# Performance work log

Hardware: AMD Instinct MI355X
Metric: run time of the kernel (lower is better)

Reference implementation:

```python
import jax, jax.numpy as jnp
import numpy as np

N = 50000          # total_nodes (B*N diagonal-stacked graphs)
E = 800000         # total edges (avg degree 16)
HID = 128          # hidden_size
HEADS = 8          # num_heads


def setup_inputs() -> dict:
    key = jax.random.key(0)
    ks = jax.random.split(key, 10)
    s = 1.0 / np.sqrt(HID)
    x = jax.random.normal(ks[0], (N, HID), jnp.float32)
    edge_index = jax.random.randint(ks[1], (2, E), 0, N, dtype=jnp.int32).astype(jnp.int64)
    Wq = jax.random.normal(ks[2], (HID, HID), jnp.float32) * s
    bq = jax.random.normal(ks[3], (HID,), jnp.float32) * 0.01
    Wk = jax.random.normal(ks[4], (HID, HID), jnp.float32) * s
    bk = jax.random.normal(ks[5], (HID,), jnp.float32) * 0.01
    Wv = jax.random.normal(ks[6], (HID, HID), jnp.float32) * s
    bv = jax.random.normal(ks[7], (HID,), jnp.float32) * 0.01
    Wo = jax.random.normal(ks[8], (HID, HID), jnp.float32) * s
    bo = jax.random.normal(ks[9], (HID,), jnp.float32) * 0.01
    return {"x": x, "edge_index": edge_index, "total_nodes": N,
            "Wq": Wq, "bq": bq, "Wk": Wk, "bk": bk,
            "Wv": Wv, "bv": bv, "Wo": Wo, "bo": bo}


def reference(x, edge_index, total_nodes, Wq, bq, Wk, bk, Wv, bv, Wo, bo):
    H = HEADS
    D = HID // HEADS
    scale = D ** (-0.5)
    # torch Linear: y = x @ W.T + b
    Q = (x @ Wq.T + bq).reshape(-1, H, D)   # (N, H, D)
    K = (x @ Wk.T + bk).reshape(-1, H, D)
    V = (x @ Wv.T + bv).reshape(-1, H, D)
    src = edge_index[0]
    dst = edge_index[1]
    # edge-wise dot-product scores: (E, H)
    scores = jnp.einsum('ehd,ehd->eh', Q[dst], K[src]) * scale
    # scatter-softmax over edges sharing the same dst node
    mx = jax.ops.segment_max(scores, dst, num_segments=total_nodes)      # (N, H)
    ex = jnp.exp(scores - mx[dst])                                        # (E, H)
    se = jax.ops.segment_sum(ex, dst, num_segments=total_nodes)          # (N, H)
    attn = ex / (se[dst] + 1e-12)                                         # (E, H)
    # weighted message aggregation
    msg = attn[..., None] * V[src]                                        # (E, H, D)
    out = jax.ops.segment_sum(msg, dst, num_segments=total_nodes)        # (N, H, D)
    out = out.reshape(total_nodes, HID)
    return out @ Wo.T + bo
```

## Files before the change

### kernel.cpp

```cpp
#include <hip/hip_runtime.h>
#include <math.h>

#define NNODES 50000
#define NEDGES 800000
#define HIDDEN 128
#define NH 8
#define HD 16
#define CAP 64
#define NPART 8
#define PART_SZ 6250
#define SCAT_BPP 128
#define SCAT_BLOCKS (NPART * SCAT_BPP)
#define QKV_BLOCKS 782

typedef __bf16 bf16x8 __attribute__((ext_vector_type(8)));
typedef float  f32x4  __attribute__((ext_vector_type(4)));

__device__ inline unsigned short f2b(float f) {
    unsigned u = __float_as_uint(f);
    unsigned r = (u + 0x7fffu + ((u >> 16) & 1u)) >> 16;
    return (unsigned short)r;
}

__device__ inline bf16x8 ld_a8(const float* __restrict__ p) {
    float4 a = *(const float4*)p;
    float4 b = *(const float4*)(p + 4);
    bf16x8 r;
    r[0] = (__bf16)a.x; r[1] = (__bf16)a.y; r[2] = (__bf16)a.z; r[3] = (__bf16)a.w;
    r[4] = (__bf16)b.x; r[5] = (__bf16)b.y; r[6] = (__bf16)b.z; r[7] = (__bf16)b.w;
    return r;
}

__device__ inline void up8(const uint4 u, float* f) {
    f[0] = __uint_as_float(u.x << 16); f[1] = __uint_as_float(u.x & 0xffff0000u);
    f[2] = __uint_as_float(u.y << 16); f[3] = __uint_as_float(u.y & 0xffff0000u);
    f[4] = __uint_as_float(u.z << 16); f[5] = __uint_as_float(u.z & 0xffff0000u);
    f[6] = __uint_as_float(u.w << 16); f[7] = __uint_as_float(u.w & 0xffff0000u);
}

__global__ __launch_bounds__(256)
void pack_init(const float* __restrict__ Wq, const float* __restrict__ Wk,
               const float* __restrict__ Wv, const float* __restrict__ Wo,
               unsigned short* __restrict__ Pqkv, unsigned short* __restrict__ Po,
               int* __restrict__ cnt)
{
    if (blockIdx.x >= 32) {
        const int idx = (blockIdx.x - 32) * 256 + threadIdx.x;
        if (idx < NNODES / 4) ((int4*)cnt)[idx] = make_int4(0, 0, 0, 0);
        return;
    }
    const int s = blockIdx.x * 4 + (threadIdx.x >> 6);
    const int lane = threadIdx.x & 63;
    const float* W; unsigned short* P; int ct, c;
    if (s < 96) { ct = s >> 2; c = s & 3;
        W = (ct < 8) ? Wq : (ct < 16) ? Wk : Wv;
        P = Pqkv + (size_t)s * 512;
        ct &= 7;
    } else { int t = s - 96; ct = t >> 2; c = t & 3; W = Wo; P = Po + (size_t)t * 512; }
    const int colin = ct * 16 + (lane & 15);
    const int k0 = c * 32 + (lane >> 4) * 8;
    const float* sp = W + (size_t)colin * 128 + k0;
    unsigned short v[8];
#pragma unroll
    for (int j = 0; j < 8; ++j) v[j] = f2b(sp[j]);
    uint4 o;
    o.x = (unsigned)v[0] | ((unsigned)v[1] << 16);
    o.y = (unsigned)v[2] | ((unsigned)v[3] << 16);
    o.z = (unsigned)v[4] | ((unsigned)v[5] << 16);
    o.w = (unsigned)v[6] | ((unsigned)v[7] << 16);
    *(uint4*)(P + lane * 8) = o;
}

__global__ __launch_bounds__(256)
void qkv_scatter(const float* __restrict__ x, const unsigned short* __restrict__ Pqkv,
                 const float* __restrict__ bq, const float* __restrict__ bk,
                 const float* __restrict__ bv,
                 const int* __restrict__ src, const int* __restrict__ dst,
                 unsigned short* __restrict__ Qb, unsigned short* __restrict__ KVb,
                 int* __restrict__ cnt, int* __restrict__ bucket)
{
    if (blockIdx.x >= QKV_BLOCKS) {
        const int sb = blockIdx.x - QKV_BLOCKS;
        const int part = sb & (NPART - 1);
        const int blk  = sb >> 3;
        const int lo = part * PART_SZ, hi = lo + PART_SZ;
        for (int e = blk * 256 + threadIdx.x; e < NEDGES; e += SCAT_BPP * 256) {
            const int d = dst[e];
            if (d >= lo && d < hi) {
                const int pos = atomicAdd(&cnt[d], 1);
                if (pos < CAP) bucket[d * CAP + pos] = src[e];
            }
        }
        return;
    }

    const int w = blockIdx.x * 4 + (threadIdx.x >> 6);
    if (w >= 3125) return;
    const int lane = threadIdx.x & 63;
    const int row0 = w * 16;
    const int ar = lane & 15, kg = lane >> 4;

    const float* ap = x + (size_t)(row0 + ar) * 128 + kg * 8;
    const bf16x8 a0 = ld_a8(ap);
    const bf16x8 a1 = ld_a8(ap + 32);
    const bf16x8 a2 = ld_a8(ap + 64);
    const bf16x8 a3 = ld_a8(ap + 96);

    const unsigned short* wp = Pqkv + lane * 8;
    bf16x8 nb0 = *(const bf16x8*)(wp);
    bf16x8 nb1 = *(const bf16x8*)(wp + 512);
    bf16x8 nb2 = *(const bf16x8*)(wp + 1024);
    bf16x8 nb3 = *(const bf16x8*)(wp + 1536);

#pragma unroll
    for (int t = 0; t < 24; ++t) {
        const bf16x8 b0 = nb0, b1 = nb1, b2 = nb2, b3 = nb3;
        if (t < 23) {
            const unsigned short* nw = wp + (size_t)(t + 1) * 2048;
            nb0 = *(const bf16x8*)(nw);
            nb1 = *(const bf16x8*)(nw + 512);
            nb2 = *(const bf16x8*)(nw + 1024);
            nb3 = *(const bf16x8*)(nw + 1536);
        }
        f32x4 acc = {0.f, 0.f, 0.f, 0.f};
        acc = __builtin_amdgcn_mfma_f32_16x16x32_bf16(a0, b0, acc, 0, 0, 0);
        acc = __builtin_amdgcn_mfma_f32_16x16x32_bf16(a1, b1, acc, 0, 0, 0);
        acc = __builtin_amdgcn_mfma_f32_16x16x32_bf16(a2, b2, acc, 0, 0, 0);
        acc = __builtin_amdgcn_mfma_f32_16x16x32_bf16(a3, b3, acc, 0, 0, 0);

        const int sel = t >> 3;
        const int colin = (t & 7) * 16 + ar;
        if (sel == 0) {
            const float bsc = bq[colin];
#pragma unroll
            for (int j = 0; j < 4; ++j)
                Qb[(size_t)(row0 + kg * 4 + j) * 128 + colin] = f2b(acc[j] + bsc);
        } else if (sel == 1) {
            const float bsc = bk[colin];
#pragma unroll
            for (int j = 0; j < 4; ++j)
                KVb[(size_t)(row0 + kg * 4 + j) * 256 + colin] = f2b(acc[j] + bsc);
        } else {
            const float bsc = bv[colin];
#pragma unroll
            for (int j = 0; j < 4; ++j)
                KVb[(size_t)(row0 + kg * 4 + j) * 256 + 128 + colin] = f2b(acc[j] + bsc);
        }
    }
}

__global__ __launch_bounds__(256)
void fused_attn_kernel(const unsigned short* __restrict__ Qb,
                       const unsigned short* __restrict__ KVb,
                       const int* __restrict__ cnt, const int* __restrict__ bucket,
                       unsigned short* __restrict__ accumb)
{
    const int wave = threadIdx.x >> 6;
    const int lane = threadIdx.x & 63;
    const int n = blockIdx.x * 4 + wave;
    if (n >= NNODES) return;

    const int h = lane >> 3;
    const int slot = lane & 7;

    int deg = cnt[n]; deg = deg > CAP ? CAP : deg;
    const int mysrc = (lane < deg) ? bucket[n * CAP + lane] : 0;

    float q[16];
    {
        const uint4* qp = (const uint4*)(Qb + (size_t)n * HIDDEN + h * 16);
        up8(qp[0], q); up8(qp[1], q + 8);
#pragma unroll
        for (int j = 0; j < 16; ++j) q[j] *= 0.25f;
    }

    float m = -1e30f, s = 0.f;
    float o[16];
#pragma unroll
    for (int j = 0; j < 16; ++j) o[j] = 0.f;

    const int nit = (deg + 7) >> 3;
    const uint4 zz = make_uint4(0, 0, 0, 0);
    uint4 k0 = zz, k1 = zz, v0 = zz, v1 = zz;
    if (slot < deg) {
        const int sid = __shfl(mysrc, slot);
        const uint4* kp = (const uint4*)(KVb + (size_t)sid * 256 + h * 16);
        k0 = kp[0]; k1 = kp[1];
        const uint4* vp = (const uint4*)(KVb + (size_t)sid * 256 + 128 + h * 16);
        v0 = vp[0]; v1 = vp[1];
    }

    for (int i = 0; i < nit; ++i) {
        uint4 nk0 = zz, nk1 = zz, nv0 = zz, nv1 = zz;
        const int nidx = i * 8 + 8 + slot;
        if (nidx < deg) {
            const int sid = __shfl(mysrc, nidx);
            const uint4* kp = (const uint4*)(KVb + (size_t)sid * 256 + h * 16);
            nk0 = kp[0]; nk1 = kp[1];
            const uint4* vp = (const uint4*)(KVb + (size_t)sid * 256 + 128 + h * 16);
            nv0 = vp[0]; nv1 = vp[1];
        }
        float kk[16], vv[16];
        up8(k0, kk); up8(k1, kk + 8);
        up8(v0, vv); up8(v1, vv + 8);

        float d0 = 0.f, d1 = 0.f, d2 = 0.f, d3 = 0.f;
#pragma unroll
        for (int j = 0; j < 16; j += 4) {
            d0 = fmaf(q[j],     kk[j],     d0);
            d1 = fmaf(q[j + 1], kk[j + 1], d1);
            d2 = fmaf(q[j + 2], kk[j + 2], d2);
            d3 = fmaf(q[j + 3], kk[j + 3], d3);
        }
        float score = (d0 + d1) + (d2 + d3);
        if (i * 8 + slot >= deg) score = -2e30f;

        const float dd = score - m;
        const float em = __expf(-fabsf(dd));
        const bool nm = dd > 0.f;
        const float so = nm ? em : 1.f;
        const float pp = nm ? 1.f : em;
        m = nm ? score : m;
        s = fmaf(s, so, pp);
#pragma unroll
        for (int j = 0; j < 16; ++j)
            o[j] = fmaf(o[j], so, pp * vv[j]);

        k0 = nk0; k1 = nk1; v0 = nv0; v1 = nv1;
    }

#pragma unroll
    for (int mask = 1; mask <= 4; mask <<= 1) {
        const float om = __shfl_xor(m, mask);
        const float dd = om - m;
        const float em = __expf(-fabsf(dd));
        const bool nm = dd > 0.f;
        const float so = nm ? em : 1.f;
        const float oo = nm ? 1.f : em;
        m = nm ? om : m;
        const float os = __shfl_xor(s, mask);
        s = fmaf(s, so, os * oo);
#pragma unroll
        for (int j = 0; j < 16; ++j) {
            const float oj = __shfl_xor(o[j], mask);
            o[j] = fmaf(o[j], so, oj * oo);
        }
    }

    if (slot == 0) {
        const float inv = 1.f / (s + 1e-12f);
        uint4 w0, w1;
        w0.x = (unsigned)f2b(o[0]  * inv) | ((unsigned)f2b(o[1]  * inv) << 16);
        w0.y = (unsigned)f2b(o[2]  * inv) | ((unsigned)f2b(o[3]  * inv) << 16);
        w0.z = (unsigned)f2b(o[4]  * inv) | ((unsigned)f2b(o[5]  * inv) << 16);
        w0.w = (unsigned)f2b(o[6]  * inv) | ((unsigned)f2b(o[7]  * inv) << 16);
        w1.x = (unsigned)f2b(o[8]  * inv) | ((unsigned)f2b(o[9]  * inv) << 16);
        w1.y = (unsigned)f2b(o[10] * inv) | ((unsigned)f2b(o[11] * inv) << 16);
        w1.z = (unsigned)f2b(o[12] * inv) | ((unsigned)f2b(o[13] * inv) << 16);
        w1.w = (unsigned)f2b(o[14] * inv) | ((unsigned)f2b(o[15] * inv) << 16);
        uint4* op = (uint4*)(accumb + (size_t)n * HIDDEN + h * 16);
        op[0] = w0; op[1] = w1;
    }
}

__global__ __launch_bounds__(256)
void outproj_mfma(const unsigned short* __restrict__ accumb, const unsigned short* __restrict__ Po,
                  const float* __restrict__ bo, float* __restrict__ out)
{
    const int band = blockIdx.x * 4 + (threadIdx.x >> 6);
    if (band >= 3125) return;
    const int lane = threadIdx.x & 63;
    const int row0 = band * 16;
    const int ar = lane & 15, kg = lane >> 4;

    const unsigned short* ab = accumb + (size_t)(row0 + ar) * 128 + kg * 8;
    const bf16x8 a0 = *(const bf16x8*)(ab);
    const bf16x8 a1 = *(const bf16x8*)(ab + 32);
    const bf16x8 a2 = *(const bf16x8*)(ab + 64);
    const bf16x8 a3 = *(const bf16x8*)(ab + 96);

    const unsigned short* wp = Po + lane * 8;
    bf16x8 nb0 = *(const bf16x8*)(wp);
    bf16x8 nb1 = *(const bf16x8*)(wp + 512);
    bf16x8 nb2 = *(const bf16x8*)(wp + 1024);
    bf16x8 nb3 = *(const bf16x8*)(wp + 1536);

#pragma unroll
    for (int t = 0; t < 8; ++t) {
        const bf16x8 b0 = nb0, b1 = nb1, b2 = nb2, b3 = nb3;
        if (t < 7) {
            const unsigned short* nw = wp + (size_t)(t + 1) * 2048;
            nb0 = *(const bf16x8*)(nw);
            nb1 = *(const bf16x8*)(nw + 512);
            nb2 = *(const bf16x8*)(nw + 1024);
            nb3 = *(const bf16x8*)(nw + 1536);
        }
        f32x4 acc = {0.f, 0.f, 0.f, 0.f};
        acc = __builtin_amdgcn_mfma_f32_16x16x32_bf16(a0, b0, acc, 0, 0, 0);
        acc = __builtin_amdgcn_mfma_f32_16x16x32_bf16(a1, b1, acc, 0, 0, 0);
        acc = __builtin_amdgcn_mfma_f32_16x16x32_bf16(a2, b2, acc, 0, 0, 0);
        acc = __builtin_amdgcn_mfma_f32_16x16x32_bf16(a3, b3, acc, 0, 0, 0);

        const int colin = t * 16 + ar;
        const float bsc = bo[colin];
#pragma unroll
        for (int j = 0; j < 4; ++j)
            out[(size_t)(row0 + kg * 4 + j) * 128 + colin] = acc[j] + bsc;
    }
}

extern "C" void kernel_launch(void* const* d_in, const int* in_sizes, int n_in,
                              void* d_out, int out_size, void* d_ws, size_t ws_size,
                              hipStream_t stream) {
    const float* x  = (const float*)d_in[0];
    const int*   ei = (const int*)d_in[1];
    const int*   src = ei;
    const int*   dst = ei + NEDGES;
    const float* Wq = (const float*)d_in[3];
    const float* bq = (const float*)d_in[4];
    const float* Wk = (const float*)d_in[5];
    const float* bk = (const float*)d_in[6];
    const float* Wv = (const float*)d_in[7];
    const float* bv = (const float*)d_in[8];
    const float* Wo = (const float*)d_in[9];
    const float* bo = (const float*)d_in[10];
    float* out = (float*)d_out;

    char* ws = (char*)d_ws;
    size_t off = 0;
    const size_t sz_nhb = (size_t)NNODES * HIDDEN * sizeof(unsigned short);
    unsigned short* Qb     = (unsigned short*)(ws + off); off += sz_nhb;
    unsigned short* KVb    = (unsigned short*)(ws + off); off += 2 * sz_nhb;
    unsigned short* accumb = (unsigned short*)(ws + off); off += sz_nhb;
    unsigned short* Pqkv   = (unsigned short*)(ws + off); off += 96 * 512 * sizeof(unsigned short);
    unsigned short* Po     = (unsigned short*)(ws + off); off += 32 * 512 * sizeof(unsigned short);
    int*            cnt    = (int*)(ws + off);            off += (size_t)NNODES * sizeof(int);
    int*            bucket = (int*)(ws + off);            off += (size_t)NNODES * CAP * sizeof(int);

    pack_init<<<81, 256, 0, stream>>>(Wq, Wk, Wv, Wo, Pqkv, Po, cnt);

    qkv_scatter<<<QKV_BLOCKS + SCAT_BLOCKS, 256, 0, stream>>>(
        x, Pqkv, bq, bk, bv, src, dst, Qb, KVb, cnt, bucket);

    fused_attn_kernel<<<(NNODES + 3) / 4, 256, 0, stream>>>(Qb, KVb, cnt, bucket, accumb);

    outproj_mfma<<<782, 256, 0, stream>>>(accumb, Po, bo, out);
}
```

Measured before the change: 137.6 us.

## Fuse attention with output projection via LDS and double rows per QKV wave

Merges the edge-attention kernel and the output-projection GEMM into one kernel. Each block computes 16 nodes' attention results, stages them as bf16 in shared memory, then runs the MFMA projection directly, which drops the accumb round trip through global memory and one launch. The QKV GEMM now processes 32 rows per wave so each loaded weight fragment is reused across two row tiles. The softmax merge across lanes is also restructured to reduce shuffles (m/s first, then scale and sum o). In exchange each wave handles four nodes serially, so per-wave latency hiding and occupancy may drop.

Result: slower. 143.5 us (+4.3%).

```diff
diff --git a/kernel.cpp b/kernel.cpp
--- a/kernel.cpp
+++ b/kernel.cpp
@@ -5,13 +5,13 @@
 #define NEDGES 800000
 #define HIDDEN 128
 #define NH 8
-#define HD 16
 #define CAP 64
 #define NPART 8
 #define PART_SZ 6250
 #define SCAT_BPP 128
 #define SCAT_BLOCKS (NPART * SCAT_BPP)
-#define QKV_BLOCKS 782
+#define QKV_WAVES 1563
+#define QKV_BLOCKS 391
 
 typedef __bf16 bf16x8 __attribute__((ext_vector_type(8)));
 typedef float  f32x4  __attribute__((ext_vector_type(4)));
@@ -95,16 +95,16 @@
     }
 
     const int w = blockIdx.x * 4 + (threadIdx.x >> 6);
-    if (w >= 3125) return;
+    if (w >= QKV_WAVES) return;
     const int lane = threadIdx.x & 63;
-    const int row0 = w * 16;
+    const int row0 = w * 32;
     const int ar = lane & 15, kg = lane >> 4;
-
-    const float* ap = x + (size_t)(row0 + ar) * 128 + kg * 8;
-    const bf16x8 a0 = ld_a8(ap);
-    const bf16x8 a1 = ld_a8(ap + 32);
-    const bf16x8 a2 = ld_a8(ap + 64);
-    const bf16x8 a3 = ld_a8(ap + 96);
+    const bool two = (row0 + 16) < NNODES;
+
+    const float* ap0 = x + (size_t)(row0 + ar) * 128 + kg * 8;
+    const float* ap1 = two ? (ap0 + 16 * 128) : ap0;
+    const bf16x8 a00 = ld_a8(ap0), a01 = ld_a8(ap0 + 32), a02 = ld_a8(ap0 + 64), a03 = ld_a8(ap0 + 96);
+    const bf16x8 a10 = ld_a8(ap1), a11 = ld_a8(ap1 + 32), a12 = ld_a8(ap1 + 64), a13 = ld_a8(ap1 + 96);
 
     const unsigned short* wp = Pqkv + lane * 8;
     bf16x8 nb0 = *(const bf16x8*)(wp);
@@ -122,190 +122,200 @@
             nb2 = *(const bf16x8*)(nw + 1024);
             nb3 = *(const bf16x8*)(nw + 1536);
         }
+        f32x4 acc0 = {0.f, 0.f, 0.f, 0.f};
+        f32x4 acc1 = {0.f, 0.f, 0.f, 0.f};
+        acc0 = __builtin_amdgcn_mfma_f32_16x16x32_bf16(a00, b0, acc0, 0, 0, 0);
+        acc1 = __builtin_amdgcn_mfma_f32_16x16x32_bf16(a10, b0, acc1, 0, 0, 0);
+        acc0 = __builtin_amdgcn_mfma_f32_16x16x32_bf16(a01, b1, acc0, 0, 0, 0);
+        acc1 = __builtin_amdgcn_mfma_f32_16x16x32_bf16(a11, b1, acc1, 0, 0, 0);
+        acc0 = __builtin_amdgcn_mfma_f32_16x16x32_bf16(a02, b2, acc0, 0, 0, 0);
+        acc1 = __builtin_amdgcn_mfma_f32_16x16x32_bf16(a12, b2, acc1, 0, 0, 0);
+        acc0 = __builtin_amdgcn_mfma_f32_16x16x32_bf16(a03, b3, acc0, 0, 0, 0);
+        acc1 = __builtin_amdgcn_mfma_f32_16x16x32_bf16(a13, b3, acc1, 0, 0, 0);
+
+        const int sel = t >> 3;
+        const int colin = (t & 7) * 16 + ar;
+        if (sel == 0) {
+            const float bsc = bq[colin];
+#pragma unroll
+            for (int j = 0; j < 4; ++j)
+                Qb[(size_t)(row0 + kg * 4 + j) * 128 + colin] = f2b(acc0[j] + bsc);
+            if (two) {
+#pragma unroll
+                for (int j = 0; j < 4; ++j)
+                    Qb[(size_t)(row0 + 16 + kg * 4 + j) * 128 + colin] = f2b(acc1[j] + bsc);
+            }
+        } else {
+            const int vo = (sel == 2) ? 128 : 0;
+            const float bsc = (sel == 1) ? bk[colin] : bv[colin];
+#pragma unroll
+            for (int j = 0; j < 4; ++j)
+                KVb[(size_t)(row0 + kg * 4 + j) * 256 + vo + colin] = f2b(acc0[j] + bsc);
+            if (two) {
+#pragma unroll
+                for (int j = 0; j < 4; ++j)
+                    KVb[(size_t)(row0 + 16 + kg * 4 + j) * 256 + vo + colin] = f2b(acc1[j] + bsc);
+            }
+        }
+    }
+}
+
+__global__ __launch_bounds__(256)
+void attn_outproj(const unsigned short* __restrict__ Qb,
+                  const unsigned short* __restrict__ KVb,
+                  const int* __restrict__ cnt, const int* __restrict__ bucket,
+                  const unsigned short* __restrict__ Po,
+                  const float* __restrict__ bo, float* __restrict__ out)
+{
+    __shared__ __align__(16) unsigned short accs[16][136];
+    const int wave = threadIdx.x >> 6;
+    const int lane = threadIdx.x & 63;
+    const int h = lane >> 3;
+    const int slot = lane & 7;
+    const int nb0 = blockIdx.x * 16;
+
+    for (int nl = 0; nl < 4; ++nl) {
+        const int n = nb0 + wave * 4 + nl;
+
+        int deg = cnt[n]; deg = deg > CAP ? CAP : deg;
+        const int mysrc = (lane < deg) ? bucket[n * CAP + lane] : 0;
+
+        float q[16];
+        {
+            const uint4* qp = (const uint4*)(Qb + (size_t)n * HIDDEN + h * 16);
+            up8(qp[0], q); up8(qp[1], q + 8);
+#pragma unroll
+            for (int j = 0; j < 16; ++j) q[j] *= 0.25f;
+        }
+
+        float m = -1e30f, s = 0.f;
+        float o[16];
+#pragma unroll
+        for (int j = 0; j < 16; ++j) o[j] = 0.f;
+
+        const int nit = (deg + 7) >> 3;
+        const uint4 zz = make_uint4(0, 0, 0, 0);
+        uint4 k0 = zz, k1 = zz, v0 = zz, v1 = zz;
+        if (slot < deg) {
+            const int sid = __shfl(mysrc, slot);
+            const uint4* kp = (const uint4*)(KVb + (size_t)sid * 256 + h * 16);
+            k0 = kp[0]; k1 = kp[1];
+            const uint4* vp = (const uint4*)(KVb + (size_t)sid * 256 + 128 + h * 16);
+            v0 = vp[0]; v1 = vp[1];
+        }
+
+        for (int i = 0; i < nit; ++i) {
+            uint4 nk0 = zz, nk1 = zz, nv0 = zz, nv1 = zz;
+            const int nidx = i * 8 + 8 + slot;
+            if (nidx < deg) {
+                const int sid = __shfl(mysrc, nidx);
+                const uint4* kp = (const uint4*)(KVb + (size_t)sid * 256 + h * 16);
+                nk0 = kp[0]; nk1 = kp[1];
+                const uint4* vp = (const uint4*)(KVb + (size_t)sid * 256 + 128 + h * 16);
+                nv0 = vp[0]; nv1 = vp[1];
+            }
+            float kk[16], vv[16];
+            up8(k0, kk); up8(k1, kk + 8);
+            up8(v0, vv); up8(v1, vv + 8);
+
+            float d0 = 0.f, d1 = 0.f, d2 = 0.f, d3 = 0.f;
+#pragma unroll
+            for (int j = 0; j < 16; j += 4) {
+                d0 = fmaf(q[j],     kk[j],     d0);
+                d1 = fmaf(q[j + 1], kk[j + 1], d1);
+                d2 = fmaf(q[j + 2], kk[j + 2], d2);
+                d3 = fmaf(q[j + 3], kk[j + 3], d3);
+            }
+            float score = (d0 + d1) + (d2 + d3);
+            if (i * 8 + slot >= deg) score = -2e30f;
+
+            const float dd = score - m;
+            const float em = __expf(-fabsf(dd));
+            const bool nm = dd > 0.f;
+            const float so = nm ? em : 1.f;
+            const float pp = nm ? 1.f : em;
+            m = nm ? score : m;
+            s = fmaf(s, so, pp);
+#pragma unroll
+            for (int j = 0; j < 16; ++j)
+                o[j] = fmaf(o[j], so, pp * vv[j]);
+
+            k0 = nk0; k1 = nk1; v0 = nv0; v1 = nv1;
+        }
+
+        float mt = m, st = s;
+#pragma unroll
+        for (int mask = 1; mask <= 4; mask <<= 1) {
+            const float om = __shfl_xor(mt, mask);
+            const float os = __shfl_xor(st, mask);
+            const float dd = om - mt;
+            const float em = __expf(-fabsf(dd));
+            const bool nm = dd > 0.f;
+            const float so = nm ? em : 1.f;
+            const float oo = nm ? 1.f : em;
+            mt = nm ? om : mt;
+            st = fmaf(st, so, os * oo);
+        }
+        const float scale = __expf(m - mt) / (st + 1e-12f);
+#pragma unroll
+        for (int j = 0; j < 16; ++j) o[j] *= scale;
+#pragma unroll
+        for (int mask = 1; mask <= 4; mask <<= 1) {
+#pragma unroll
+            for (int j = 0; j < 16; ++j) o[j] += __shfl_xor(o[j], mask);
+        }
+
+        if (slot == 0) {
+            const int nloc = wave * 4 + nl;
+            uint4 w0, w1;
+            w0.x = (unsigned)f2b(o[0])  | ((unsigned)f2b(o[1])  << 16);
+            w0.y = (unsigned)f2b(o[2])  | ((unsigned)f2b(o[3])  << 16);
+            w0.z = (unsigned)f2b(o[4])  | ((unsigned)f2b(o[5])  << 16);
+            w0.w = (unsigned)f2b(o[6])  | ((unsigned)f2b(o[7])  << 16);
+            w1.x = (unsigned)f2b(o[8])  | ((unsigned)f2b(o[9])  << 16);
+            w1.y = (unsigned)f2b(o[10]) | ((unsigned)f2b(o[11]) << 16);
+            w1.z = (unsigned)f2b(o[12]) | ((unsigned)f2b(o[13]) << 16);
+            w1.w = (unsigned)f2b(o[14]) | ((unsigned)f2b(o[15]) << 16);
+            *(uint4*)&accs[nloc][h * 16]     = w0;
+            *(uint4*)&accs[nloc][h * 16 + 8] = w1;
+        }
+    }
+    __syncthreads();
+
+    const int ar = lane & 15, kg = lane >> 4;
+    const unsigned short* ab = &accs[ar][kg * 8];
+    const bf16x8 a0 = *(const bf16x8*)(ab);
+    const bf16x8 a1 = *(const bf16x8*)(ab + 32);
+    const bf16x8 a2 = *(const bf16x8*)(ab + 64);
+    const bf16x8 a3 = *(const bf16x8*)(ab + 96);
+
+    const unsigned short* wp = Po + lane * 8;
+    bf16x8 pb0 = *(const bf16x8*)(wp);
+    bf16x8 pb1 = *(const bf16x8*)(wp + 512);
+    bf16x8 pb2 = *(const bf16x8*)(wp + 1024);
+    bf16x8 pb3 = *(const bf16x8*)(wp + 1536);
+
+#pragma unroll
+    for (int t = 0; t < 8; ++t) {
+        const bf16x8 b0 = pb0, b1 = pb1, b2 = pb2, b3 = pb3;
+        if (t < 7) {
+            const unsigned short* nw = wp + (size_t)(t + 1) * 2048;
+            pb0 = *(const bf16x8*)(nw);
+            pb1 = *(const bf16x8*)(nw + 512);
+            pb2 = *(const bf16x8*)(nw + 1024);
+            pb3 = *(const bf16x8*)(nw + 1536);
+        }
         f32x4 acc = {0.f, 0.f, 0.f, 0.f};
         acc = __builtin_amdgcn_mfma_f32_16x16x32_bf16(a0, b0, acc, 0, 0, 0);
         acc = __builtin_amdgcn_mfma_f32_16x16x32_bf16(a1, b1, acc, 0, 0, 0);
         acc = __builtin_amdgcn_mfma_f32_16x16x32_bf16(a2, b2, acc, 0, 0, 0);
         acc = __builtin_amdgcn_mfma_f32_16x16x32_bf16(a3, b3, acc, 0, 0, 0);
 
-        const int sel = t >> 3;
-        const int colin = (t & 7) * 16 + ar;
-        if (sel == 0) {
-            const float bsc = bq[colin];
-#pragma unroll
-            for (int j = 0; j < 4; ++j)
-                Qb[(size_t)(row0 + kg * 4 + j) * 128 + colin] = f2b(acc[j] + bsc);
-        } else if (sel == 1) {
-            const float bsc = bk[colin];
-#pragma unroll
-            for (int j = 0; j < 4; ++j)
-                KVb[(size_t)(row0 + kg * 4 + j) * 256 + colin] = f2b(acc[j] + bsc);
-        } else {
-            const float bsc = bv[colin];
-#pragma unroll
-            for (int j = 0; j < 4; ++j)
-                KVb[(size_t)(row0 + kg * 4 + j) * 256 + 128 + colin] = f2b(acc[j] + bsc);
-        }
-    }
-}
-
-__global__ __launch_bounds__(256)
-void fused_attn_kernel(const unsigned short* __restrict__ Qb,
-                       const unsigned short* __restrict__ KVb,
-                       const int* __restrict__ cnt, const int* __restrict__ bucket,
-                       unsigned short* __restrict__ accumb)
-{
-    const int wave = threadIdx.x >> 6;
-    const int lane = threadIdx.x & 63;
-    const int n = blockIdx.x * 4 + wave;
-    if (n >= NNODES) return;
-
-    const int h = lane >> 3;
-    const int slot = lane & 7;
-
-    int deg = cnt[n]; deg = deg > CAP ? CAP : deg;
-    const int mysrc = (lane < deg) ? bucket[n * CAP + lane] : 0;
-
-    float q[16];
-    {
-        const uint4* qp = (const uint4*)(Qb + (size_t)n * HIDDEN + h * 16);
-        up8(qp[0], q); up8(qp[1], q + 8);
-#pragma unroll
-        for (int j = 0; j < 16; ++j) q[j] *= 0.25f;
-    }
-
-    float m = -1e30f, s = 0.f;
-    float o[16];
-#pragma unroll
-    for (int j = 0; j < 16; ++j) o[j] = 0.f;
-
-    const int nit = (deg + 7) >> 3;
-    const uint4 zz = make_uint4(0, 0, 0, 0);
-    uint4 k0 = zz, k1 = zz, v0 = zz, v1 = zz;
-    if (slot < deg) {
-        const int sid = __shfl(mysrc, slot);
-        const uint4* kp = (const uint4*)(KVb + (size_t)sid * 256 + h * 16);
-        k0 = kp[0]; k1 = kp[1];
-        const uint4* vp = (const uint4*)(KVb + (size_t)sid * 256 + 128 + h * 16);
-        v0 = vp[0]; v1 = vp[1];
-    }
-
-    for (int i = 0; i < nit; ++i) {
-        uint4 nk0 = zz, nk1 = zz, nv0 = zz, nv1 = zz;
-        const int nidx = i * 8 + 8 + slot;
-        if (nidx < deg) {
-            const int sid = __shfl(mysrc, nidx);
-            const uint4* kp = (const uint4*)(KVb + (size_t)sid * 256 + h * 16);
-            nk0 = kp[0]; nk1 = kp[1];
-            const uint4* vp = (const uint4*)(KVb + (size_t)sid * 256 + 128 + h * 16);
-            nv0 = vp[0]; nv1 = vp[1];
-        }
-        float kk[16], vv[16];
-        up8(k0, kk); up8(k1, kk + 8);
-        up8(v0, vv); up8(v1, vv + 8);
-
-        float d0 = 0.f, d1 = 0.f, d2 = 0.f, d3 = 0.f;
-#pragma unroll
-        for (int j = 0; j < 16; j += 4) {
-            d0 = fmaf(q[j],     kk[j],     d0);
-            d1 = fmaf(q[j + 1], kk[j + 1], d1);
-            d2 = fmaf(q[j + 2], kk[j + 2], d2);
-            d3 = fmaf(q[j + 3], kk[j + 3], d3);
-        }
-        float score = (d0 + d1) + (d2 + d3);
-        if (i * 8 + slot >= deg) score = -2e30f;
-
-        const float dd = score - m;
-        const float em = __expf(-fabsf(dd));
-        const bool nm = dd > 0.f;
-        const float so = nm ? em : 1.f;
-        const float pp = nm ? 1.f : em;
-        m = nm ? score : m;
-        s = fmaf(s, so, pp);
-#pragma unroll
-        for (int j = 0; j < 16; ++j)
-            o[j] = fmaf(o[j], so, pp * vv[j]);
-
-        k0 = nk0; k1 = nk1; v0 = nv0; v1 = nv1;
-    }
-
-#pragma unroll
-    for (int mask = 1; mask <= 4; mask <<= 1) {
-        const float om = __shfl_xor(m, mask);
-        const float dd = om - m;
-        const float em = __expf(-fabsf(dd));
-        const bool nm = dd > 0.f;
-        const float so = nm ? em : 1.f;
-        const float oo = nm ? 1.f : em;
-        m = nm ? om : m;
-        const float os = __shfl_xor(s, mask);
-        s = fmaf(s, so, os * oo);
-#pragma unroll
-        for (int j = 0; j < 16; ++j) {
-            const float oj = __shfl_xor(o[j], mask);
-            o[j] = fmaf(o[j], so, oj * oo);
-        }
-    }
-
-    if (slot == 0) {
-        const float inv = 1.f / (s + 1e-12f);
-        uint4 w0, w1;
-        w0.x = (unsigned)f2b(o[0]  * inv) | ((unsigned)f2b(o[1]  * inv) << 16);
-        w0.y = (unsigned)f2b(o[2]  * inv) | ((unsigned)f2b(o[3]  * inv) << 16);
-        w0.z = (unsigned)f2b(o[4]  * inv) | ((unsigned)f2b(o[5]  * inv) << 16);
-        w0.w = (unsigned)f2b(o[6]  * inv) | ((unsigned)f2b(o[7]  * inv) << 16);
-        w1.x = (unsigned)f2b(o[8]  * inv) | ((unsigned)f2b(o[9]  * inv) << 16);
-        w1.y = (unsigned)f2b(o[10] * inv) | ((unsigned)f2b(o[11] * inv) << 16);
-        w1.z = (unsigned)f2b(o[12] * inv) | ((unsigned)f2b(o[13] * inv) << 16);
-        w1.w = (unsigned)f2b(o[14] * inv) | ((unsigned)f2b(o[15] * inv) << 16);
-        uint4* op = (uint4*)(accumb + (size_t)n * HIDDEN + h * 16);
-        op[0] = w0; op[1] = w1;
-    }
-}
-
-__global__ __launch_bounds__(256)
-void outproj_mfma(const unsigned short* __restrict__ accumb, const unsigned short* __restrict__ Po,
-                  const float* __restrict__ bo, float* __restrict__ out)
-{
-    const int band = blockIdx.x * 4 + (threadIdx.x >> 6);
-    if (band >= 3125) return;
-    const int lane = threadIdx.x & 63;
-    const int row0 = band * 16;
-    const int ar = lane & 15, kg = lane >> 4;
-
-    const unsigned short* ab = accumb + (size_t)(row0 + ar) * 128 + kg * 8;
-    const bf16x8 a0 = *(const bf16x8*)(ab);
-    const bf16x8 a1 = *(const bf16x8*)(ab + 32);
-    const bf16x8 a2 = *(const bf16x8*)(ab + 64);
-    const bf16x8 a3 = *(const bf16x8*)(ab + 96);
-
-    const unsigned short* wp = Po + lane * 8;
-    bf16x8 nb0 = *(const bf16x8*)(wp);
-    bf16x8 nb1 = *(const bf16x8*)(wp + 512);
-    bf16x8 nb2 = *(const bf16x8*)(wp + 1024);
-    bf16x8 nb3 = *(const bf16x8*)(wp + 1536);
-
-#pragma unroll
-    for (int t = 0; t < 8; ++t) {
-        const bf16x8 b0 = nb0, b1 = nb1, b2 = nb2, b3 = nb3;
-        if (t < 7) {
-            const unsigned short* nw = wp + (size_t)(t + 1) * 2048;
-            nb0 = *(const bf16x8*)(nw);
-            nb1 = *(const bf16x8*)(nw + 512);
-            nb2 = *(const bf16x8*)(nw + 1024);
-            nb3 = *(const bf16x8*)(nw + 1536);
-        }
-        f32x4 acc = {0.f, 0.f, 0.f, 0.f};
-        acc = __builtin_amdgcn_mfma_f32_16x16x32_bf16(a0, b0, acc, 0, 0, 0);
-        acc = __builtin_amdgcn_mfma_f32_16x16x32_bf16(a1, b1, acc, 0, 0, 0);
-        acc = __builtin_amdgcn_mfma_f32_16x16x32_bf16(a2, b2, acc, 0, 0, 0);
-        acc = __builtin_amdgcn_mfma_f32_16x16x32_bf16(a3, b3, acc, 0, 0, 0);
-
         const int colin = t * 16 + ar;
         const float bsc = bo[colin];
 #pragma unroll
         for (int j = 0; j < 4; ++j)
-            out[(size_t)(row0 + kg * 4 + j) * 128 + colin] = acc[j] + bsc;
+            out[(size_t)(nb0 + kg * 4 + j) * 128 + colin] = acc[j] + bsc;
     }
 }
 
@@ -331,7 +341,6 @@
     const size_t sz_nhb = (size_t)NNODES * HIDDEN * sizeof(unsigned short);
     unsigned short* Qb     = (unsigned short*)(ws + off); off += sz_nhb;
     unsigned short* KVb    = (unsigned short*)(ws + off); off += 2 * sz_nhb;
-    unsigned short* accumb = (unsigned short*)(ws + off); off += sz_nhb;
     unsigned short* Pqkv   = (unsigned short*)(ws + off); off += 96 * 512 * sizeof(unsigned short);
     unsigned short* Po     = (unsigned short*)(ws + off); off += 32 * 512 * sizeof(unsigned short);
     int*            cnt    = (int*)(ws + off);            off += (size_t)NNODES * sizeof(int);
@@ -342,7 +351,5 @@
     qkv_scatter<<<QKV_BLOCKS + SCAT_BLOCKS, 256, 0, stream>>>(
         x, Pqkv, bq, bk, bv, src, dst, Qb, KVb, cnt, bucket);
 
-    fused_attn_kernel<<<(NNODES + 3) / 4, 256, 0, stream>>>(Qb, KVb, cnt, bucket, accumb);
-
-    outproj_mfma<<<782, 256, 0, stream>>>(accumb, Po, bo, out);
-}
+    attn_outproj<<<3125, 256, 0, stream>>>(Qb, KVb, cnt, bucket, Po, bo, out);
+}
```
